# Kernel optimization log

Hardware: AMD Instinct MI355X
Metric: run time of the kernel (lower is better)

## Reference

```python
import jax, jax.numpy as jnp
import numpy as np
from math import comb

# --- module hyperparameters (from init_kwargs / module-level constants) ---
F = 32          # features
NITER = 3       # num_iterations
NB = 16         # num_basis_functions
NDCM = 4        # n_dcm
CUTOFF = 4.0
MAXZ = 17       # max_atomic_number
NC = 9          # (max_degree+1)^2 spherical components, max_degree=2
DEG = np.array([0, 1, 1, 1, 2, 2, 2, 2, 2])  # degree l of each component
BINOM = jnp.asarray([comb(NB - 1, k) for k in range(NB)], dtype=jnp.float32)


def _np_sph9(x, y, z):
    # real spherical harmonics up to l=2 on the unit sphere (numpy, for Gaunt table)
    c0 = 0.28209479177387814; c1 = 0.4886025119029199
    c2a = 1.0925484305920792; c2b = 0.31539156525252005; c2c = 0.5462742152960396
    return np.stack([c0 * np.ones_like(x), c1 * y, c1 * z, c1 * x,
                     c2a * x * y, c2a * y * z, c2b * (3.0 * z * z - 1.0),
                     c2a * x * z, c2c * (x * x - y * y)], axis=0)


def _gaunt():
    # real Gaunt (Clebsch-Gordan-type) coefficients G[a,b,c] = int Y_a Y_b Y_c dOmega
    # via Gauss-Legendre (cos theta) x midpoint (phi) quadrature -- exact for l<=2 products
    ct, wt = np.polynomial.legendre.leggauss(64)
    nph = 256
    phi = (np.arange(nph) + 0.5) * (2.0 * np.pi / nph)
    st = np.sqrt(1.0 - ct ** 2)
    x = st[:, None] * np.cos(phi)[None, :]
    y = st[:, None] * np.sin(phi)[None, :]
    z = np.broadcast_to(ct[:, None], x.shape)
    w = (wt[:, None] * (2.0 * np.pi / nph)) * np.ones((1, nph))
    Y = _np_sph9(x, y, z)
    G = np.einsum('aij,bij,cij,ij->abc', Y, Y, Y, w)
    G[np.abs(G) < 1e-6] = 0.0
    return G

CG = jnp.asarray(_gaunt(), dtype=jnp.float32)  # (9, 9, 9), sparse


def _sph9(u):
    # u: (E, 3) unit vectors -> (E, 9)
    x, y, z = u[:, 0], u[:, 1], u[:, 2]
    c0 = 0.28209479177387814; c1 = 0.4886025119029199
    c2a = 1.0925484305920792; c2b = 0.31539156525252005; c2c = 0.5462742152960396
    return jnp.stack([jnp.full_like(x, c0), c1 * y, c1 * z, c1 * x,
                      c2a * x * y, c2a * y * z, c2b * (3.0 * z * z - 1.0),
                      c2a * x * z, c2c * (x * x - y * y)], axis=-1)


def _radial(r):
    # reciprocal Bernstein radial basis * smooth cutoff; r: (E,) -> (E, NB)
    u = 1.0 / (1.0 + r)
    k = jnp.arange(NB, dtype=jnp.float32)
    rb = BINOM * u[:, None] ** k * (1.0 - u[:, None]) ** (NB - 1 - k)
    t = r / CUTOFF
    den = jnp.where(t < 1.0, 1.0 - t * t, 1.0)
    fc = jnp.where(t < 1.0, jnp.exp(-t * t / den), 0.0)  # smooth_cutoff
    return rb * fc[:, None]


def _equiv_dense(x, W, b=None):
    # per-degree linear (equivariant Dense): x (N, 9, Fin), W (3, Fin, Fout); bias on l=0 only
    y = jnp.einsum('ncf,cfg->ncg', x, W[DEG])
    if b is not None:
        y = y.at[:, 0, :].add(b)
    return y


def _tp(xs, bf):
    # Gaunt tensor-product contraction: out[e,c,f] = sum_ab CG[a,b,c] xs[e,a,f] bf[e,b,f]
    # loop over the 9 fixed output components to avoid an (E,9,9,F) intermediate
    out = []
    for c in range(NC):
        t = jnp.einsum('eaf,ab->ebf', xs, CG[:, :, c])
        out.append(jnp.sum(t * bf, axis=1))
    return jnp.stack(out, axis=1)


def _forward(atomic_numbers, positions, dst_idx, src_idx, embed, Wb, W1, b1, W2, b2,
             Wt00, Wt11, Wmono, element_bias):
    n = atomic_numbers.shape[0]
    disp = positions[src_idx] - positions[dst_idx]                 # (E, 3) gather
    r = jnp.sqrt(jnp.sum(disp * disp, axis=-1) + 1e-12)            # safe norm
    u = disp / r[:, None]
    basis = _sph9(u)[:, :, None] * _radial(r)[:, None, :]          # (E, 9, NB)
    x = jnp.zeros((n, NC, F), dtype=positions.dtype).at[:, 0, :].set(embed[atomic_numbers])
    for i in range(NITER):  # message passing iterations
        bf = jnp.einsum('ebn,bng->ebg', basis, Wb[i][DEG])         # per-degree radial->feature mix (E,9,F)
        msg = _tp(x[src_idx], bf)                                  # gather src + tensor product
        y = x + jax.ops.segment_sum(msg, dst_idx, num_segments=n)  # scatter-aggregate + residual add
        y = _equiv_dense(y, W1[i], b1[i])
        y = jax.nn.silu(y)
        y = _equiv_dense(y, W2[i], b2[i])
        x = x + y                                                  # residual update
    # TensorDense to n_dcm channels, then readout heads
    mono = (x[:, 0, :] @ Wt00) @ Wmono + element_bias[atomic_numbers][:, None]  # (N, NDCM)
    dip = jnp.einsum('ncf,fg->ncg', x[:, 1:4, :], Wt11)            # (N, 3, NDCM) vector channel
    dip = jnp.clip(jax.nn.silu(dip), -0.3, 0.3) + positions[:, :, None]
    return mono, dip


def setup_inputs():
    key = jax.random.key(0)
    ks = jax.random.split(key, 12)
    N, E = 10000, 160000
    return {
        'atomic_numbers': jax.random.randint(ks[0], (N,), 0, MAXZ + 1),
        'positions': jax.random.normal(ks[1], (N, 3), jnp.float32) * 3.0,
        'dst_idx': jax.random.randint(ks[2], (E,), 0, N),
        'src_idx': jax.random.randint(ks[3], (E,), 0, N),
        'embed': jax.random.normal(ks[4], (MAXZ + 1, F), jnp.float32),
        'Wb': jax.random.normal(ks[5], (NITER, 3, NB, F), jnp.float32) / np.sqrt(NB).astype(np.float32),
        'W1': jax.random.normal(ks[6], (NITER, 3, F, F), jnp.float32) / np.sqrt(F).astype(np.float32),
        'b1': jnp.zeros((NITER, F), jnp.float32),
        'W2': jax.random.normal(ks[7], (NITER, 3, F, F), jnp.float32) / np.sqrt(F).astype(np.float32),
        'b2': jnp.zeros((NITER, F), jnp.float32),
        'Wt00': jax.random.normal(ks[8], (F, NDCM), jnp.float32) / np.sqrt(F).astype(np.float32),
        'Wt11': jax.random.normal(ks[9], (F, NDCM), jnp.float32) / np.sqrt(F).astype(np.float32),
        'Wmono': jax.random.normal(ks[10], (NDCM, NDCM), jnp.float32) / np.sqrt(NDCM).astype(np.float32),
        'element_bias': jnp.zeros((MAXZ + 1,), jnp.float32),
    }


def reference(atomic_numbers, positions, dst_idx, src_idx, embed, Wb, W1, b1, W2, b2,
              Wt00, Wt11, Wmono, element_bias):
    return _forward(atomic_numbers, positions, dst_idx, src_idx, embed, Wb, W1, b1, W2, b2,
                    Wt00, Wt11, Wmono, element_bias)
```

## Files before the change

kernel.cpp:

```cpp
#include <hip/hip_runtime.h>
#include <hip/hip_bf16.h>


#define NITER 3
#define BCAP  64

#define OFF_WB    0
#define OFF_W1    4608
#define OFF_B1    13824
#define OFF_W2    13920
#define OFF_B2    23136
#define OFF_WT00  23232
#define OFF_WT11  23360
#define OFF_WMONO 23488
#define OFF_EB    23504
#define OFF_EMB   23522
#define WC_TOTAL  24098

__device__ __forceinline__ float b2f(const __hip_bfloat16 v) { return __bfloat162float(v); }

#define KC0 0.28209479177387814f
#define KG1 0.21850968611841584f
#define KG2 0.12615662610100802f
#define KG3 0.18022375157287861f
// ... 17 lines not shown
}

__device__ __forceinline__ float xadd32(float v) {
    return v + __int_as_float(__shfl_xor(__float_as_int(v), 32, 64));
}

__device__ __forceinline__ bool edge_geom(float dx, float dy, float dz,
                                          float* sp, float* rad) {
    float r2 = dx*dx + dy*dy + dz*dz + 1e-12f;
    if (r2 >= 16.0f) return false;
    float r  = sqrtf(r2);
    float t2 = r2 * 0.0625f;
    float fc = __expf(-t2 / (1.0f - t2));
    float u = 1.0f / (1.0f + r);
    float v = 1.0f - u;
    const float BIN[16] = {1.f,15.f,105.f,455.f,1365.f,3003.f,5005.f,6435.f,
                           6435.f,5005.f,3003.f,1365.f,455.f,105.f,15.f,1.f};
    float vp[16];
    vp[0] = 1.0f;
    #pragma unroll
    for (int k = 1; k < 16; k++) vp[k] = vp[k-1] * v;
    float up = 1.0f;
    #pragma unroll
    for (int n = 0; n < 16; n++) { rad[n] = BIN[n] * up * vp[15-n] * fc; up *= u; }
    float ir = 1.0f / r;
    float ux = dx*ir, uy = dy*ir, uz = dz*ir;
    const float c0 = 0.28209479177387814f, c1 = 0.4886025119029199f;
    const float c2a = 1.0925484305920792f, c2b = 0.31539156525252005f, c2c = 0.5462742152960396f;
    sp[0] = c0;
    sp[1] = c1*uy; sp[2] = c1*uz; sp[3] = c1*ux;
    sp[4] = c2a*ux*uy; sp[5] = c2a*uy*uz; sp[6] = c2b*(3.0f*uz*uz - 1.0f);
    sp[7] = c2a*ux*uz; sp[8] = c2c*(ux*ux - uy*uy);
    return true;
}

__global__ void setup_kernel(const void* pos, const void* Wb, const void* W1,
        const void* b1, const void* W2, const void* b2, const void* Wt00,
        const void* Wt11, const void* Wmono, const void* eb, const void* emb,
        const int* __restrict__ an,
        const int* __restrict__ srcI, const int* __restrict__ dstI,
        float* __restrict__ posf, float* __restrict__ wc,
        float* __restrict__ x, float* __restrict__ geo2, int* __restrict__ cur,
        int N, int E, int use_csr) {
    bool f32 = wave_sniff(pos);
    int i = blockIdx.x * blockDim.x + threadIdx.x;
    int np = N * 3;
    if (i < np) { posf[i] = ldany(pos, i, f32); return; }
    int j = i - np;
    if (j < WC_TOTAL) {
        const void* src; int rel;
        if      (j < OFF_W1)    { src = Wb;    rel = j; }
        else if (j < OFF_B1)    { src = W1;    rel = j - OFF_W1; }
        else if (j < OFF_W2)    { src = b1;    rel = j - OFF_B1; }
        else if (j < OFF_B2)    { src = W2;    rel = j - OFF_W2; }
        else if (j < OFF_WT00)  { src = b2;    rel = j - OFF_B2; }
        else if (j < OFF_WT11)  { src = Wt00;  rel = j - OFF_WT00; }
        else if (j < OFF_WMONO) { src = Wt11;  rel = j - OFF_WT11; }
        else if (j < OFF_EB)    { src = Wmono; rel = j - OFF_WMONO; }
        else if (j < OFF_EMB)   { src = eb;    rel = j - OFF_EB; }
        else                    { src = emb;   rel = j - OFF_EMB; }
        wc[j] = ldany(src, rel, f32);
        return;
    }
    j -= WC_TOTAL;
    if (j < N * 32) {
        int n = j >> 5, rem = j & 31;
        x[(size_t)n * 288 + rem] = ldany(emb, an[n] * 32 + rem, f32);
        return;
    }
    j -= N * 32;
    if (j < E && use_csr) {
        int s = srcI[j], d = dstI[j];
        float sp[9], rad[16];
        if (!edge_geom(ldany(pos, s*3+0, f32) - ldany(pos, d*3+0, f32),
                       ldany(pos, s*3+1, f32) - ldany(pos, d*3+1, f32),
                       ldany(pos, s*3+2, f32) - ldany(pos, d*3+2, f32),
                       sp, rad)) return;
        int slot = atomicAdd(&cur[d], 1);
        float* gp = geo2 + ((size_t)d * BCAP + slot) * 32;
        gp[0] = __int_as_float(s);
        gp[1] = 0.0f;
        #pragma unroll
        for (int a = 0; a < 9; a++) gp[2 + a] = sp[a];
        gp[11] = 0.0f;
        #pragma unroll
        for (int k = 0; k < 16; k++) gp[16 + k] = rad[k];
    }
}

template <bool FIRST, bool LAST>
__global__ __launch_bounds__(256) void edge_gather_kernel(
        const float* __restrict__ x, float* __restrict__ y,
        const float* __restrict__ geo2, const int* __restrict__ cur,
        const float* __restrict__ Wbi, int N) {
    int tid  = threadIdx.x;
    int f    = tid & 31;
    int half = (tid >> 5) & 1;
    int n    = (blockIdx.x * blockDim.x + tid) >> 6;
    if (n >= N) return;
    float w0[16], w1[16], w2[16];
    #pragma unroll
    for (int k = 0; k < 16; k++) {
        w0[k] = Wbi[(0*16 + k)*32 + f];
        w1[k] = Wbi[(1*16 + k)*32 + f];
        w2[k] = Wbi[(2*16 + k)*32 + f];
    }
    float A0=0.f,A1=0.f,A2=0.f,A3=0.f,A4=0.f,A5=0.f,A6=0.f,A7=0.f,A8=0.f;
    int beg = n * BCAP, end = beg + cur[n];
    for (int e = beg + half; e < end; e += 2) {
        const float4* gp = (const float4*)(geo2 + (size_t)e * 32);
        float4 h0 = gp[0], h1 = gp[1], h2 = gp[2];
        float4 r0 = gp[4], r1 = gp[5], r2 = gp[6], r3 = gp[7];
        int s = __float_as_int(h0.x);
        float rad[16] = {r0.x,r0.y,r0.z,r0.w, r1.x,r1.y,r1.z,r1.w,
                         r2.x,r2.y,r2.z,r2.w, r3.x,r3.y,r3.z,r3.w};
        float rw0 = 0.f, rw1 = 0.f, rw2 = 0.f;
        #pragma unroll
        for (int k = 0; k < 16; k++) {
            rw0 = fmaf(rad[k], w0[k], rw0);
            rw1 = fmaf(rad[k], w1[k], rw1);
            rw2 = fmaf(rad[k], w2[k], rw2);
        }
        float B0 = h0.z*rw0;
        float B1 = h0.w*rw1, B2 = h1.x*rw1, B3 = h1.y*rw1;
        float B4 = h1.z*rw2, B5 = h1.w*rw2, B6 = h2.x*rw2,
              B7 = h2.y*rw2, B8 = h2.z*rw2;
        const float* xp = x + (size_t)s*288 + f;
        if (FIRST) {
            float X0 = xp[0];
            float k0 = KC0 * X0;
            A0 += k0*B0; A1 += k0*B1; A2 += k0*B2; A3 += k0*B3; A4 += k0*B4;
            A5 += k0*B5; A6 += k0*B6; A7 += k0*B7; A8 += k0*B8;
        } else {
            float X0 = xp[0],   X1 = xp[32],  X2 = xp[64],  X3 = xp[96],  X4 = xp[128];
            float X5 = xp[160], X6 = xp[192], X7 = xp[224], X8 = xp[256];
            A0 += KC0*(X0*B0 + X1*B1 + X2*B2 + X3*B3 + X4*B4 + X5*B5 + X6*B6 + X7*B7 + X8*B8);
            A1 += KC0*(X0*B1 + X1*B0) + KG1*(X3*B4 + X4*B3 + X2*B5 + X5*B2)
                - KG2*(X1*B6 + X6*B1) - KG1*(X1*B8 + X8*B1);
            A2 += KC0*(X0*B2 + X2*B0) + KG1*(X1*B5 + X5*B1 + X3*B7 + X7*B3)
                + 2.0f*KG2*(X2*B6 + X6*B2);
            A3 += KC0*(X0*B3 + X3*B0) + KG1*(X1*B4 + X4*B1 + X2*B7 + X7*B2)
                - KG2*(X3*B6 + X6*B3) + KG1*(X3*B8 + X8*B3);
            if (!LAST) {
                A4 += KC0*(X0*B4 + X4*B0) + KG1*(X1*B3 + X3*B1) + KG5*(X5*B7 + X7*B5)
                    - KG3*(X4*B6 + X6*B4);
                A5 += KC0*(X0*B5 + X5*B0) + KG1*(X1*B2 + X2*B1) + KG5*(X4*B7 + X7*B4)
                    + KG4*(X5*B6 + X6*B5) - KG5*(X5*B8 + X8*B5);
                A6 += KC0*(X0*B6 + X6*B0) - KG2*X1*B1 + 2.0f*KG2*X2*B2 - KG2*X3*B3
                    - KG3*X4*B4 + KG4*X5*B5 + KG3*X6*B6 + KG4*X7*B7 - KG3*X8*B8;
                A7 += KC0*(X0*B7 + X7*B0) + KG1*(X2*B3 + X3*B2) + KG5*(X4*B5 + X5*B4)
                    + KG4*(X6*B7 + X7*B6) + KG5*(X7*B8 + X8*B7);
                A8 += KC0*(X0*B8 + X8*B0) - KG1*X1*B1 + KG1*X3*B3 - KG5*X5*B5 + KG5*X7*B7
                    - KG3*(X6*B8 + X8*B6);
            }
        }
    }
    A0 = xadd32(A0); A1 = xadd32(A1); A2 = xadd32(A2); A3 = xadd32(A3);
    if (!LAST) {
        A4 = xadd32(A4); A5 = xadd32(A5); A6 = xadd32(A6);
        A7 = xadd32(A7); A8 = xadd32(A8);
    }
    if (half == 0) {
        float* yp = y + (size_t)n * 288 + f;
        yp[0]   = A0; yp[32]  = A1; yp[64]  = A2; yp[96]  = A3;
        if (!LAST) {
            yp[128] = A4; yp[160] = A5; yp[192] = A6; yp[224] = A7; yp[256] = A8;
        }
    }
}

template <bool FIRST>
__global__ __launch_bounds__(256) void atom_kernel(
        float* __restrict__ x, const float* __restrict__ y,
        const float* __restrict__ W1i, const float* __restrict__ b1i,
        const float* __restrict__ W2i, const float* __restrict__ b2i,
        int N) {
    __shared__ float sm[4][64*33];
    int lane  = threadIdx.x & 63;
    int wslot = threadIdx.x >> 6;
    int u = __builtin_amdgcn_readfirstlane(blockIdx.x * 4 + wslot);
    int t = u / 9;
    int c = u - t * 9;
    int d = (c == 0) ? 0 : ((c < 4) ? 1 : 2);
    const float* W1 = W1i + d * 1024;
    const float* W2 = W2i + d * 1024;
    float* tile = sm[wslot];
    bool usex = (!FIRST) || (c == 0);
    float4 xr4[8];
    #pragma unroll
    for (int k = 0; k < 8; k++) {
        int e  = lane * 4 + k * 256;
        int al = e >> 5, f = e & 31;
        int ag = t * 64 + al;
        float4 s = make_float4(0.f, 0.f, 0.f, 0.f);
        float4 xv = make_float4(0.f, 0.f, 0.f, 0.f);
        if (ag < N) {
            if (usex) xv = *(const float4*)(x + (size_t)ag * 288 + c * 32 + f);
            float4 yv = *(const float4*)(y + (size_t)ag * 288 + c * 32 + f);
            s = make_float4(xv.x + yv.x, xv.y + yv.y, xv.z + yv.z, xv.w + yv.w);
        }
        xr4[k] = xv;
        *(float4*)(tile + al * 33 + f) = s;
    }
    __syncthreads();
    float yin[32];
    #pragma unroll
    for (int k = 0; k < 8; k++) {
        float4 v = *(const float4*)(tile + lane * 33 + 4 * k);
        yin[4*k+0] = v.x; yin[4*k+1] = v.y; yin[4*k+2] = v.z; yin[4*k+3] = v.w;
    }
    float acc[32];
    #pragma unroll
    for (int g = 0; g < 32; g++) acc[g] = (c == 0) ? b1i[g] : 0.0f;
    #pragma unroll 4
    for (int fi = 0; fi < 32; fi++) {
        float v = yin[fi];
        #pragma unroll
        for (int g = 0; g < 32; g++) acc[g] = fmaf(v, W1[fi*32 + g], acc[g]);
    }
    #pragma unroll
    for (int g = 0; g < 32; g++)
        acc[g] = acc[g] * __builtin_amdgcn_rcpf(1.0f + __expf(-acc[g]));
    float out[32];
    #pragma unroll
    for (int g = 0; g < 32; g++) out[g] = (c == 0) ? b2i[g] : 0.0f;
    #pragma unroll 4
    for (int fi = 0; fi < 32; fi++) {
        float v = acc[fi];
        #pragma unroll
        for (int g = 0; g < 32; g++) out[g] = fmaf(v, W2[fi*32 + g], out[g]);
    }
    __syncthreads();
    #pragma unroll
    for (int k = 0; k < 8; k++)
        *(float4*)(tile + lane * 33 + 4 * k) =
            make_float4(out[4*k+0], out[4*k+1], out[4*k+2], out[4*k+3]);
    __syncthreads();
    #pragma unroll
    for (int k = 0; k < 8; k++) {
        int e  = lane * 4 + k * 256;
        int al = e >> 5, f = e & 31;
        int ag = t * 64 + al;
        if (ag < N) {
            float4 dv = *(const float4*)(tile + al * 33 + f);
            float4 xv = xr4[k];
            *(float4*)(x + (size_t)ag * 288 + c * 32 + f) =
                make_float4(xv.x + dv.x, xv.y + dv.y, xv.z + dv.z, xv.w + dv.w);
        }
    }
}

__global__ __launch_bounds__(256) void atom_readout_kernel(
        const float* __restrict__ x, const float* __restrict__ y,
        const float* __restrict__ W1i, const float* __restrict__ b1i,
        const float* __restrict__ W2i, const float* __restrict__ b2i,
        const int* __restrict__ an, const float* __restrict__ posf,
        const float* __restrict__ wc, const void* __restrict__ pos,
        void* __restrict__ out_, int N) {
    bool f32 = wave_sniff(pos);
    __shared__ float sm[4][64*33];
    int lane  = threadIdx.x & 63;
    int wslot = threadIdx.x >> 6;
    int c = __builtin_amdgcn_readfirstlane(wslot);
    int t = blockIdx.x;
    int d = (c == 0) ? 0 : 1;
    const float* W1 = W1i + d * 1024;
    const float* W2 = W2i + d * 1024;
    float* tile = sm[wslot];
    float4 xr4[8];
    #pragma unroll
    for (int k = 0; k < 8; k++) {
        int e  = lane * 4 + k * 256;
        int al = e >> 5, f = e & 31;
        int ag = t * 64 + al;
        float4 s = make_float4(0.f, 0.f, 0.f, 0.f);
        float4 xv = make_float4(0.f, 0.f, 0.f, 0.f);
        if (ag < N) {
            xv = *(const float4*)(x + (size_t)ag * 288 + c * 32 + f);
            float4 yv = *(const float4*)(y + (size_t)ag * 288 + c * 32 + f);
            s = make_float4(xv.x + yv.x, xv.y + yv.y, xv.z + yv.z, xv.w + yv.w);
        }
        xr4[k] = xv;
        *(float4*)(tile + al * 33 + f) = s;
    }
    __syncthreads();
    float yin[32];
    #pragma unroll
    for (int k = 0; k < 8; k++) {
        float4 v = *(const float4*)(tile + lane * 33 + 4 * k);
        yin[4*k+0] = v.x; yin[4*k+1] = v.y; yin[4*k+2] = v.z; yin[4*k+3] = v.w;
    }
    float acc[32];
    #pragma unroll
    for (int g = 0; g < 32; g++) acc[g] = (c == 0) ? b1i[g] : 0.0f;
    #pragma unroll 4
    for (int fi = 0; fi < 32; fi++) {
        float v = yin[fi];
        #pragma unroll
        for (int g = 0; g < 32; g++) acc[g] = fmaf(v, W1[fi*32 + g], acc[g]);
    }
    #pragma unroll
    for (int g = 0; g < 32; g++)
        acc[g] = acc[g] * __builtin_amdgcn_rcpf(1.0f + __expf(-acc[g]));
    float out[32];
    #pragma unroll
    for (int g = 0; g < 32; g++) out[g] = (c == 0) ? b2i[g] : 0.0f;
    #pragma unroll 4
    for (int fi = 0; fi < 32; fi++) {
        float v = acc[fi];
        #pragma unroll
        for (int g = 0; g < 32; g++) out[g] = fmaf(v, W2[fi*32 + g], out[g]);
    }
    __syncthreads();
    #pragma unroll
    for (int k = 0; k < 8; k++)
        *(float4*)(tile + lane * 33 + 4 * k) =
            make_float4(out[4*k+0], out[4*k+1], out[4*k+2], out[4*k+3]);
    __syncthreads();
    #pragma unroll
    for (int k = 0; k < 8; k++) {
        int e  = lane * 4 + k * 256;
        int al = e >> 5, f = e & 31;
        float4 dv = *(const float4*)(tile + al * 33 + f);
        float4 xv = xr4[k];
        *(float4*)(tile + al * 33 + f) =
            make_float4(xv.x + dv.x, xv.y + dv.y, xv.z + dv.z, xv.w + dv.w);
    }
    __syncthreads();
    if (threadIdx.x < 64) {
        int a  = threadIdx.x;
        int ag = t * 64 + a;
        if (ag < N) {
            const float* Wt00  = wc + OFF_WT00;
            const float* Wt11  = wc + OFF_WT11;
            const float* Wmono = wc + OFF_WMONO;
            const float* x0 = sm[0] + a * 33;
            float q[4] = {0.f, 0.f, 0.f, 0.f};
            for (int f = 0; f < 32; f++) {
                float xv = x0[f];
                #pragma unroll
                for (int j = 0; j < 4; j++) q[j] = fmaf(xv, Wt00[f*4 + j], q[j]);
            }
            float ebv = wc[OFF_EB + an[ag]];
            #pragma unroll
            for (int m = 0; m < 4; m++) {
                float accm = ebv;
                #pragma unroll
                for (int j = 0; j < 4; j++) accm = fmaf(q[j], Wmono[j*4 + m], accm);
                if (f32) ((float*)out_)[ag*4 + m] = accm;
                else ((__hip_bfloat16*)out_)[ag*4 + m] = __float2bfloat16(accm);
            }
            #pragma unroll
            for (int cc = 0; cc < 3; cc++) {
                float pc = posf[ag*3 + cc];
                const float* xc = sm[1 + cc] + a * 33;
                float dq[4] = {0.f, 0.f, 0.f, 0.f};
                for (int f = 0; f < 32; f++) {
                    float xv = xc[f];
                    #pragma unroll
                    for (int m = 0; m < 4; m++) dq[m] = fmaf(xv, Wt11[f*4 + m], dq[m]);
                }
                #pragma unroll
                for (int m = 0; m < 4; m++) {
                    float v = dq[m];
                    v = v * __builtin_amdgcn_rcpf(1.0f + __expf(-v));
                    v = fminf(fmaxf(v, -0.3f), 0.3f);
                    v += pc;
                    if (f32) ((float*)out_)[N*4 + ag*12 + cc*4 + m] = v;
                    else ((__hip_bfloat16*)out_)[N*4 + ag*12 + cc*4 + m] = __float2bfloat16(v);
                }
            }
        }
    }
}

__global__ void zero_kernel(float4* __restrict__ b, int n) {
    int i = blockIdx.x * blockDim.x + threadIdx.x;
    int stride = gridDim.x * blockDim.x;
    float4 z = make_float4(0.f, 0.f, 0.f, 0.f);
    for (; i < n; i += stride) b[i] = z;
}

__global__ __launch_bounds__(256) void edge_inline_kernel(
        const float* __restrict__ x, float* __restrict__ y,
        const float* __restrict__ posf,
        const int* __restrict__ srcI, const int* __restrict__ dstI,
        const float* __restrict__ Wbi, int E) {
    int f  = threadIdx.x & 31;
    int hw = (blockIdx.x * blockDim.x + threadIdx.x) >> 5;
    int nhw = gridDim.x * (blockDim.x >> 5);
    float w0[16], w1[16], w2[16];
    #pragma unroll
    for (int n = 0; n < 16; n++) {
        w0[n] = Wbi[(0*16 + n)*32 + f];
        w1[n] = Wbi[(1*16 + n)*32 + f];
        w2[n] = Wbi[(2*16 + n)*32 + f];
    }
    for (int e = hw; e < E; e += nhw) {
        int s = srcI[e], d = dstI[e];
        float sp[9], rad[16];
        if (!edge_geom(posf[s*3+0] - posf[d*3+0],
                       posf[s*3+1] - posf[d*3+1],
                       posf[s*3+2] - posf[d*3+2], sp, rad)) continue;
        float rw0 = 0.f, rw1 = 0.f, rw2 = 0.f;
        #pragma unroll
        for (int n = 0; n < 16; n++) {
// ... 77 lines not shown
        }
        #pragma unroll
        for (int m = 0; m < 4; m++) {
            float v = dq[m];
            v = v * __builtin_amdgcn_rcpf(1.0f + __expf(-v));
            v = fminf(fmaxf(v, -0.3f), 0.3f);
            v += pc;
            if (f32) ((float*)out)[N*4 + n*12 + c*4 + m] = v;
            else ((__hip_bfloat16*)out)[N*4 + n*12 + c*4 + m] = __float2bfloat16(v);
        }
    }
}

extern "C" void kernel_launch(void* const* d_in, const int* in_sizes, int n_in,
                              void* d_out, int out_size, void* d_ws, size_t ws_size,
                              hipStream_t stream) {
    const int* an    = (const int*)d_in[0];
    const void* pos  = d_in[1];
    const int* dstI  = (const int*)d_in[2];
    const int* srcI  = (const int*)d_in[3];
    const void* embed= d_in[4];
    const void* Wb   = d_in[5];
    const void* W1   = d_in[6];
    const void* b1   = d_in[7];
    const void* W2   = d_in[8];
    const void* b2   = d_in[9];
    const void* Wt00 = d_in[10];
    const void* Wt11 = d_in[11];
    const void* Wmono= d_in[12];
    const void* eb   = d_in[13];
    int N = in_sizes[0];
    int E = in_sizes[2];

    float* x    = (float*)d_ws;
    float* y    = x + (size_t)N * 288;
    float* posf = y + (size_t)N * 288;
    float* wc   = posf + (size_t)N * 3;
    int* cur    = (int*)(wc + WC_TOTAL);
    uintptr_t ga = ((uintptr_t)(cur + N) + 127) & ~(uintptr_t)127;
    float* geo2 = (float*)ga;
    size_t need = (uintptr_t)(geo2 + (size_t)N * BCAP * 32) - (uintptr_t)d_ws;
    bool use_csr = (ws_size >= need);

    hipMemsetAsync(cur, 0, sizeof(int) * (size_t)N, stream);
    if (!use_csr)
        zero_kernel<<<512, 256, 0, stream>>>((float4*)x, N * 72);
    {
        int tot = N * 3 + WC_TOTAL + N * 32 + (use_csr ? E : 0);
        setup_kernel<<<(tot + 255)/256, 256, 0, stream>>>(
            pos, Wb, W1, b1, W2, b2, Wt00, Wt11, Wmono, eb, embed,
            an, srcI, dstI, posf, wc, x, geo2, cur, N, E, use_csr ? 1 : 0);
    }
    int ntiles = (N + 63) / 64;
    if (use_csr) {
        int gblocks = (N + 3) / 4;
        for (int i = 0; i < NITER; i++) {
            const float* Wbi = wc + OFF_WB + (size_t)i*1536;
            const float* W1i = wc + OFF_W1 + (size_t)i*3072;
            const float* b1i = wc + OFF_B1 + (size_t)i*32;
            const float* W2i = wc + OFF_W2 + (size_t)i*3072;
            const float* b2i = wc + OFF_B2 + (size_t)i*32;
            if (i == 0) {
                edge_gather_kernel<true,false><<<gblocks, 256, 0, stream>>>(
                    x, y, geo2, cur, Wbi, N);
                atom_kernel<true><<<(ntiles*9 + 3)/4, 256, 0, stream>>>(
                    x, y, W1i, b1i, W2i, b2i, N);
            } else if (i == NITER - 1) {
                edge_gather_kernel<false,true><<<gblocks, 256, 0, stream>>>(
                    x, y, geo2, cur, Wbi, N);
                atom_readout_kernel<<<ntiles, 256, 0, stream>>>(
                    x, y, W1i, b1i, W2i, b2i, an, posf, wc, pos, d_out, N);
            } else {
                edge_gather_kernel<false,false><<<gblocks, 256, 0, stream>>>(
                    x, y, geo2, cur, Wbi, N);
                atom_kernel<false><<<(ntiles*9 + 3)/4, 256, 0, stream>>>(
                    x, y, W1i, b1i, W2i, b2i, N);
            }
        }
    } else {
        int ablocks = (ntiles * 9 + 3) / 4;
        for (int i = 0; i < NITER; i++) {
            zero_kernel<<<512, 256, 0, stream>>>((float4*)y, N * 72);
            edge_inline_kernel<<<2048, 256, 0, stream>>>(x, y, posf, srcI, dstI,
                wc + OFF_WB + (size_t)i*1536, E);
            atom_kernel<false><<<ablocks, 256, 0, stream>>>(x, y,
                wc + OFF_W1 + (size_t)i*3072, wc + OFF_B1 + (size_t)i*32,
                wc + OFF_W2 + (size_t)i*3072, wc + OFF_B2 + (size_t)i*32, N);
        }
        readout_kernel<<<(N + 255)/256, 256, 0, stream>>>(x, an, posf, wc, pos,
                                                          d_out, N);
    }
}
```

Before: 212.2 us.

## Fuse edge gather and atom MLP into one per-iteration kernel with ping-pong buffers

Replaces the separate edge_gather and atom kernels in the CSR path with a single iter_kernel per iteration. Each wavefront gathers messages for one atom, adds the residual, and runs the two 32x32 MLPs from a shared-memory tile. The last iteration also computes the readout directly. Features ping-pong between two buffers so the y intermediate array is never written or re-read, and three launches plus their global round-trips are removed. In exchange, each 64-lane wave now does the MLP work for one atom, reading weights per channel instead of using the earlier 64-atom tiled matmul, so MLP weight reuse is lower.

New measurement: 224.1 us. +5.6%, slower.

```diff
diff --git a/kernel.cpp b/kernel.cpp
--- a/kernel.cpp
+++ b/kernel.cpp
@@ -73,6 +73,214 @@
     sp[4] = c2a*ux*uy; sp[5] = c2a*uy*uz; sp[6] = c2b*(3.0f*uz*uz - 1.0f);
     sp[7] = c2a*ux*uz; sp[8] = c2c*(ux*ux - uy*uy);
     return true;
+}
+
+__device__ __forceinline__ void write_geo_slot(float* gp, int s,
+                                               const float* sp, const float* rad) {
+    float4* g4 = (float4*)gp;
+    g4[0] = make_float4(__int_as_float(s), 0.f, sp[0], sp[1]);
+    g4[1] = make_float4(sp[2], sp[3], sp[4], sp[5]);
+    g4[2] = make_float4(sp[6], sp[7], sp[8], 0.f);
+    g4[4] = make_float4(rad[0],  rad[1],  rad[2],  rad[3]);
+    g4[5] = make_float4(rad[4],  rad[5],  rad[6],  rad[7]);
+    g4[6] = make_float4(rad[8],  rad[9],  rad[10], rad[11]);
+    g4[7] = make_float4(rad[12], rad[13], rad[14], rad[15]);
+}
+
+template <bool FIRST, bool LAST>
+__global__ __launch_bounds__(256) void iter_kernel(
+        const float* __restrict__ xin, float* __restrict__ xout,
+        const float* __restrict__ geo2, const int* __restrict__ cur,
+        const float* __restrict__ Wbi,
+        const float* __restrict__ W1i, const float* __restrict__ b1i,
+        const float* __restrict__ W2i, const float* __restrict__ b2i,
+        const int* __restrict__ an, const float* __restrict__ posf,
+        const float* __restrict__ wc, const void* __restrict__ pos,
+        void* __restrict__ out_, int N) {
+    constexpr int NCH = LAST ? 4 : 9;
+    constexpr int NR  = LAST ? 2 : 5;
+    __shared__ float sm[4][9][33];
+    bool f32o = false;
+    if (LAST) f32o = wave_sniff(pos);
+    int tid   = threadIdx.x;
+    int wslot = tid >> 6;
+    int lane  = tid & 63;
+    int f     = lane & 31;
+    int half  = lane >> 5;
+    int n     = blockIdx.x * 4 + wslot;
+    bool act  = (n < N);
+    float (*tile)[33] = sm[wslot];
+
+    float w0[16], w1[16], w2[16];
+    #pragma unroll
+    for (int k = 0; k < 16; k++) {
+        w0[k] = Wbi[(0*16 + k)*32 + f];
+        w1[k] = Wbi[(1*16 + k)*32 + f];
+        w2[k] = Wbi[(2*16 + k)*32 + f];
+    }
+    float A0=0.f,A1=0.f,A2=0.f,A3=0.f,A4=0.f,A5=0.f,A6=0.f,A7=0.f,A8=0.f;
+    if (act) {
+        int beg = n * BCAP, end = beg + cur[n];
+        for (int e = beg + half; e < end; e += 2) {
+            const float4* gp = (const float4*)(geo2 + (size_t)e * 32);
+            float4 h0 = gp[0], h1 = gp[1], h2 = gp[2];
+            float4 r0 = gp[4], r1 = gp[5], r2 = gp[6], r3 = gp[7];
+            int s = __float_as_int(h0.x);
+            float rad[16] = {r0.x,r0.y,r0.z,r0.w, r1.x,r1.y,r1.z,r1.w,
+                             r2.x,r2.y,r2.z,r2.w, r3.x,r3.y,r3.z,r3.w};
+            float rw0 = 0.f, rw1 = 0.f, rw2 = 0.f;
+            #pragma unroll
+            for (int k = 0; k < 16; k++) {
+                rw0 = fmaf(rad[k], w0[k], rw0);
+                rw1 = fmaf(rad[k], w1[k], rw1);
+                rw2 = fmaf(rad[k], w2[k], rw2);
+            }
+            float B0 = h0.z*rw0;
+            float B1 = h0.w*rw1, B2 = h1.x*rw1, B3 = h1.y*rw1;
+            float B4 = h1.z*rw2, B5 = h1.w*rw2, B6 = h2.x*rw2,
+                  B7 = h2.y*rw2, B8 = h2.z*rw2;
+            const float* xp = xin + (size_t)s*288 + f;
+            if (FIRST) {
+                float X0 = xp[0];
+                float k0 = KC0 * X0;
+                A0 += k0*B0; A1 += k0*B1; A2 += k0*B2; A3 += k0*B3; A4 += k0*B4;
+                A5 += k0*B5; A6 += k0*B6; A7 += k0*B7; A8 += k0*B8;
+            } else {
+                float X0 = xp[0],   X1 = xp[32],  X2 = xp[64],  X3 = xp[96],  X4 = xp[128];
+                float X5 = xp[160], X6 = xp[192], X7 = xp[224], X8 = xp[256];
+                A0 += KC0*(X0*B0 + X1*B1 + X2*B2 + X3*B3 + X4*B4 + X5*B5 + X6*B6 + X7*B7 + X8*B8);
+                A1 += KC0*(X0*B1 + X1*B0) + KG1*(X3*B4 + X4*B3 + X2*B5 + X5*B2)
+                    - KG2*(X1*B6 + X6*B1) - KG1*(X1*B8 + X8*B1);
+                A2 += KC0*(X0*B2 + X2*B0) + KG1*(X1*B5 + X5*B1 + X3*B7 + X7*B3)
+                    + 2.0f*KG2*(X2*B6 + X6*B2);
+                A3 += KC0*(X0*B3 + X3*B0) + KG1*(X1*B4 + X4*B1 + X2*B7 + X7*B2)
+                    - KG2*(X3*B6 + X6*B3) + KG1*(X3*B8 + X8*B3);
+                if (!LAST) {
+                    A4 += KC0*(X0*B4 + X4*B0) + KG1*(X1*B3 + X3*B1) + KG5*(X5*B7 + X7*B5)
+                        - KG3*(X4*B6 + X6*B4);
+                    A5 += KC0*(X0*B5 + X5*B0) + KG1*(X1*B2 + X2*B1) + KG5*(X4*B7 + X7*B4)
+                        + KG4*(X5*B6 + X6*B5) - KG5*(X5*B8 + X8*B5);
+                    A6 += KC0*(X0*B6 + X6*B0) - KG2*X1*B1 + 2.0f*KG2*X2*B2 - KG2*X3*B3
+                        - KG3*X4*B4 + KG4*X5*B5 + KG3*X6*B6 + KG4*X7*B7 - KG3*X8*B8;
+                    A7 += KC0*(X0*B7 + X7*B0) + KG1*(X2*B3 + X3*B2) + KG5*(X4*B5 + X5*B4)
+                        + KG4*(X6*B7 + X7*B6) + KG5*(X7*B8 + X8*B7);
+                    A8 += KC0*(X0*B8 + X8*B0) - KG1*X1*B1 + KG1*X3*B3 - KG5*X5*B5 + KG5*X7*B7
+                        - KG3*(X6*B8 + X8*B6);
+                }
+            }
+        }
+    }
+    A0 = xadd32(A0); A1 = xadd32(A1); A2 = xadd32(A2); A3 = xadd32(A3);
+    if (!LAST) {
+        A4 = xadd32(A4); A5 = xadd32(A5); A6 = xadd32(A6);
+        A7 = xadd32(A7); A8 = xadd32(A8);
+    }
+
+    float xr[9];
+    #pragma unroll
+    for (int c = 0; c < 9; c++) xr[c] = 0.f;
+    if (act) {
+        if (FIRST) {
+            xr[0] = xin[(size_t)n*288 + f];
+        } else {
+            #pragma unroll
+            for (int c = 0; c < NCH; c++) xr[c] = xin[(size_t)n*288 + c*32 + f];
+        }
+    }
+
+    if (act && half == 0) {
+        tile[0][f] = xr[0] + A0;
+        tile[1][f] = xr[1] + A1;
+        tile[2][f] = xr[2] + A2;
+        tile[3][f] = xr[3] + A3;
+        if (!LAST) {
+            tile[4][f] = xr[4] + A4;
+            tile[5][f] = xr[5] + A5;
+            tile[6][f] = xr[6] + A6;
+            tile[7][f] = xr[7] + A7;
+            tile[8][f] = xr[8] + A8;
+        }
+    }
+    __syncthreads();
+
+    int g = f;
+    float o1[NR];
+    #pragma unroll
+    for (int cc = 0; cc < NR; cc++) {
+        int c  = cc*2 + half;
+        int cs = (c < NCH) ? c : 0;
+        int d  = (cs == 0) ? 0 : ((cs < 4) ? 1 : 2);
+        const float* W1p = W1i + d * 1024;
+        float acc = (c == 0) ? b1i[g] : 0.f;
+        #pragma unroll
+        for (int fi = 0; fi < 32; fi++)
+            acc = fmaf(tile[cs][fi], W1p[fi*32 + g], acc);
+        acc = acc * __builtin_amdgcn_rcpf(1.0f + __expf(-acc));
+        o1[cc] = acc;
+    }
+    __syncthreads();
+    #pragma unroll
+    for (int cc = 0; cc < NR; cc++) {
+        int c = cc*2 + half;
+        if (c < NCH) tile[c][g] = o1[cc];
+    }
+    __syncthreads();
+
+    #pragma unroll
+    for (int cc = 0; cc < NR; cc++) {
+        int c  = cc*2 + half;
+        int cs = (c < NCH) ? c : 0;
+        int d  = (cs == 0) ? 0 : ((cs < 4) ? 1 : 2);
+        const float* W2p = W2i + d * 1024;
+        float acc = (c == 0) ? b2i[g] : 0.f;
+        #pragma unroll
+        for (int fi = 0; fi < 32; fi++)
+            acc = fmaf(tile[cs][fi], W2p[fi*32 + g], acc);
+        float xf = xr[cs] + acc;
+        if (!LAST) {
+            if (act && c < NCH)
+                xout[(size_t)n*288 + c*32 + g] = xf;
+        } else if (act) {
+            const float* WT = (c == 0) ? (wc + OFF_WT00) : (wc + OFF_WT11);
+            float p0 = xf * WT[g*4 + 0];
+            float p1 = xf * WT[g*4 + 1];
+            float p2 = xf * WT[g*4 + 2];
+            float p3 = xf * WT[g*4 + 3];
+            #pragma unroll
+            for (int m = 1; m <= 16; m <<= 1) {
+                p0 += __shfl_xor(p0, m, 64);
+                p1 += __shfl_xor(p1, m, 64);
+                p2 += __shfl_xor(p2, m, 64);
+                p3 += __shfl_xor(p3, m, 64);
+            }
+            if (g == 0) {
+                if (c == 0) {
+                    const float* Wmono = wc + OFF_WMONO;
+                    float ebv = wc[OFF_EB + an[n]];
+                    #pragma unroll
+                    for (int m = 0; m < 4; m++) {
+                        float a2 = ebv + p0*Wmono[0*4+m] + p1*Wmono[1*4+m]
+                                       + p2*Wmono[2*4+m] + p3*Wmono[3*4+m];
+                        if (f32o) ((float*)out_)[n*4 + m] = a2;
+                        else ((__hip_bfloat16*)out_)[n*4 + m] = __float2bfloat16(a2);
+                    }
+                } else {
+                    float pc = posf[n*3 + (c - 1)];
+                    float pv[4] = {p0, p1, p2, p3};
+                    #pragma unroll
+                    for (int m = 0; m < 4; m++) {
+                        float v = pv[m];
+                        v = v * __builtin_amdgcn_rcpf(1.0f + __expf(-v));
+                        v = fminf(fmaxf(v, -0.3f), 0.3f);
+                        v += pc;
+                        size_t o = (size_t)N*4 + (size_t)n*12 + (size_t)(c-1)*4 + m;
+                        if (f32o) ((float*)out_)[o] = v;
+                        else ((__hip_bfloat16*)out_)[o] = __float2bfloat16(v);
+                    }
+                }
+            }
+        }
+    }
 }
 
 __global__ void setup_kernel(const void* pos, const void* Wb, const void* W1,
@@ -118,94 +326,81 @@
                        ldany(pos, s*3+2, f32) - ldany(pos, d*3+2, f32),
                        sp, rad)) return;
         int slot = atomicAdd(&cur[d], 1);
-        float* gp = geo2 + ((size_t)d * BCAP + slot) * 32;
-        gp[0] = __int_as_float(s);
-        gp[1] = 0.0f;
-        #pragma unroll
-        for (int a = 0; a < 9; a++) gp[2 + a] = sp[a];
-        gp[11] = 0.0f;
-        #pragma unroll
-        for (int k = 0; k < 16; k++) gp[16 + k] = rad[k];
-    }
-}
-
-template <bool FIRST, bool LAST>
-__global__ __launch_bounds__(256) void edge_gather_kernel(
-        const float* __restrict__ x, float* __restrict__ y,
-        const float* __restrict__ geo2, const int* __restrict__ cur,
-        const float* __restrict__ Wbi, int N) {
-    int tid  = threadIdx.x;
-    int f    = tid & 31;
-    int half = (tid >> 5) & 1;
-    int n    = (blockIdx.x * blockDim.x + tid) >> 6;
-    if (n >= N) return;
-    float w0[16], w1[16], w2[16];
-    #pragma unroll
-    for (int k = 0; k < 16; k++) {
-        w0[k] = Wbi[(0*16 + k)*32 + f];
-        w1[k] = Wbi[(1*16 + k)*32 + f];
-        w2[k] = Wbi[(2*16 + k)*32 + f];
-    }
-    float A0=0.f,A1=0.f,A2=0.f,A3=0.f,A4=0.f,A5=0.f,A6=0.f,A7=0.f,A8=0.f;
-    int beg = n * BCAP, end = beg + cur[n];
-    for (int e = beg + half; e < end; e += 2) {
-        const float4* gp = (const float4*)(geo2 + (size_t)e * 32);
-        float4 h0 = gp[0], h1 = gp[1], h2 = gp[2];
-        float4 r0 = gp[4], r1 = gp[5], r2 = gp[6], r3 = gp[7];
-        int s = __float_as_int(h0.x);
-        float rad[16] = {r0.x,r0.y,r0.z,r0.w, r1.x,r1.y,r1.z,r1.w,
-                         r2.x,r2.y,r2.z,r2.w, r3.x,r3.y,r3.z,r3.w};
-        float rw0 = 0.f, rw1 = 0.f, rw2 = 0.f;
-        #pragma unroll
-        for (int k = 0; k < 16; k++) {
-            rw0 = fmaf(rad[k], w0[k], rw0);
-            rw1 = fmaf(rad[k], w1[k], rw1);
-            rw2 = fmaf(rad[k], w2[k], rw2);
-        }
-        float B0 = h0.z*rw0;
-        float B1 = h0.w*rw1, B2 = h1.x*rw1, B3 = h1.y*rw1;
-        float B4 = h1.z*rw2, B5 = h1.w*rw2, B6 = h2.x*rw2,
-              B7 = h2.y*rw2, B8 = h2.z*rw2;
-        const float* xp = x + (size_t)s*288 + f;
-        if (FIRST) {
-            float X0 = xp[0];
-            float k0 = KC0 * X0;
-            A0 += k0*B0; A1 += k0*B1; A2 += k0*B2; A3 += k0*B3; A4 += k0*B4;
-            A5 += k0*B5; A6 += k0*B6; A7 += k0*B7; A8 += k0*B8;
-        } else {
-            float X0 = xp[0],   X1 = xp[32],  X2 = xp[64],  X3 = xp[96],  X4 = xp[128];
-            float X5 = xp[160], X6 = xp[192], X7 = xp[224], X8 = xp[256];
-            A0 += KC0*(X0*B0 + X1*B1 + X2*B2 + X3*B3 + X4*B4 + X5*B5 + X6*B6 + X7*B7 + X8*B8);
-            A1 += KC0*(X0*B1 + X1*B0) + KG1*(X3*B4 + X4*B3 + X2*B5 + X5*B2)
-                - KG2*(X1*B6 + X6*B1) - KG1*(X1*B8 + X8*B1);
-            A2 += KC0*(X0*B2 + X2*B0) + KG1*(X1*B5 + X5*B1 + X3*B7 + X7*B3)
-                + 2.0f*KG2*(X2*B6 + X6*B2);
-            A3 += KC0*(X0*B3 + X3*B0) + KG1*(X1*B4 + X4*B1 + X2*B7 + X7*B2)
-                - KG2*(X3*B6 + X6*B3) + KG1*(X3*B8 + X8*B3);
-            if (!LAST) {
-                A4 += KC0*(X0*B4 + X4*B0) + KG1*(X1*B3 + X3*B1) + KG5*(X5*B7 + X7*B5)
-                    - KG3*(X4*B6 + X6*B4);
-                A5 += KC0*(X0*B5 + X5*B0) + KG1*(X1*B2 + X2*B1) + KG5*(X4*B7 + X7*B4)
-                    + KG4*(X5*B6 + X6*B5) - KG5*(X5*B8 + X8*B5);
-                A6 += KC0*(X0*B6 + X6*B0) - KG2*X1*B1 + 2.0f*KG2*X2*B2 - KG2*X3*B3
-                    - KG3*X4*B4 + KG4*X5*B5 + KG3*X6*B6 + KG4*X7*B7 - KG3*X8*B8;
-                A7 += KC0*(X0*B7 + X7*B0) + KG1*(X2*B3 + X3*B2) + KG5*(X4*B5 + X5*B4)
-                    + KG4*(X6*B7 + X7*B6) + KG5*(X7*B8 + X8*B7);
-                A8 += KC0*(X0*B8 + X8*B0) - KG1*X1*B1 + KG1*X3*B3 - KG5*X5*B5 + KG5*X7*B7
-                    - KG3*(X6*B8 + X8*B6);
-            }
-        }
-    }
-    A0 = xadd32(A0); A1 = xadd32(A1); A2 = xadd32(A2); A3 = xadd32(A3);
-    if (!LAST) {
-        A4 = xadd32(A4); A5 = xadd32(A5); A6 = xadd32(A6);
-        A7 = xadd32(A7); A8 = xadd32(A8);
-    }
-    if (half == 0) {
-        float* yp = y + (size_t)n * 288 + f;
-        yp[0]   = A0; yp[32]  = A1; yp[64]  = A2; yp[96]  = A3;
-        if (!LAST) {
-            yp[128] = A4; yp[160] = A5; yp[192] = A6; yp[224] = A7; yp[256] = A8;
+        write_geo_slot(geo2 + ((size_t)d * BCAP + slot) * 32, s, sp, rad);
+    }
+}
+
+template <bool FIRST>
+__device__ __forceinline__ void atom_unit(
+        const float* __restrict__ xin, float* __restrict__ xout,
+        const float* __restrict__ y,
+        const float* __restrict__ W1i, const float* __restrict__ b1i,
+        const float* __restrict__ W2i, const float* __restrict__ b2i,
+        int N, int t, int c, int lane, float* __restrict__ tile) {
+    int d = (c == 0) ? 0 : ((c < 4) ? 1 : 2);
+    const float* W1 = W1i + d * 1024;
+    const float* W2 = W2i + d * 1024;
+    bool usex = (!FIRST) || (c == 0);
+    float4 xr4[8];
+    #pragma unroll
+    for (int k = 0; k < 8; k++) {
+        int e  = lane * 4 + k * 256;
+        int al = e >> 5, f = e & 31;
+        int ag = t * 64 + al;
+        float4 s = make_float4(0.f, 0.f, 0.f, 0.f);
+        float4 xv = make_float4(0.f, 0.f, 0.f, 0.f);
+        if (ag < N) {
+            if (usex) xv = *(const float4*)(xin + (size_t)ag * 288 + c * 32 + f);
+            float4 yv = *(const float4*)(y + (size_t)ag * 288 + c * 32 + f);
+            s = make_float4(xv.x + yv.x, xv.y + yv.y, xv.z + yv.z, xv.w + yv.w);
+        }
+        xr4[k] = xv;
+        *(float4*)(tile + al * 33 + f) = s;
+    }
+    __syncthreads();
+    float yin[32];
+    #pragma unroll
+    for (int k = 0; k < 8; k++) {
+        float4 v = *(const float4*)(tile + lane * 33 + 4 * k);
+        yin[4*k+0] = v.x; yin[4*k+1] = v.y; yin[4*k+2] = v.z; yin[4*k+3] = v.w;
+    }
+    float acc[32];
+    #pragma unroll
+    for (int g = 0; g < 32; g++) acc[g] = (c == 0) ? b1i[g] : 0.0f;
+    #pragma unroll 4
+    for (int fi = 0; fi < 32; fi++) {
+        float v = yin[fi];
+        #pragma unroll
+        for (int g = 0; g < 32; g++) acc[g] = fmaf(v, W1[fi*32 + g], acc[g]);
+    }
+    #pragma unroll
+    for (int g = 0; g < 32; g++)
+        acc[g] = acc[g] * __builtin_amdgcn_rcpf(1.0f + __expf(-acc[g]));
+    float out[32];
+    #pragma unroll
+    for (int g = 0; g < 32; g++) out[g] = (c == 0) ? b2i[g] : 0.0f;
+    #pragma unroll 4
+    for (int fi = 0; fi < 32; fi++) {
+        float v = acc[fi];
+        #pragma unroll
+        for (int g = 0; g < 32; g++) out[g] = fmaf(v, W2[fi*32 + g], out[g]);
+    }
+    __syncthreads();
+    #pragma unroll
+    for (int k = 0; k < 8; k++)
+        *(float4*)(tile + lane * 33 + 4 * k) =
+            make_float4(out[4*k+0], out[4*k+1], out[4*k+2], out[4*k+3]);
+    __syncthreads();
+    #pragma unroll
+    for (int k = 0; k < 8; k++) {
+        int e  = lane * 4 + k * 256;
+        int al = e >> 5, f = e & 31;
+        int ag = t * 64 + al;
+        if (ag < N) {
+            float4 dv = *(const float4*)(tile + al * 33 + f);
+            float4 xv = xr4[k];
+            *(float4*)(xout + (size_t)ag * 288 + c * 32 + f) =
+                make_float4(xv.x + dv.x, xv.y + dv.y, xv.z + dv.z, xv.w + dv.w);
         }
     }
 }
@@ -222,197 +417,7 @@
     int u = __builtin_amdgcn_readfirstlane(blockIdx.x * 4 + wslot);
     int t = u / 9;
     int c = u - t * 9;
-    int d = (c == 0) ? 0 : ((c < 4) ? 1 : 2);
-    const float* W1 = W1i + d * 1024;
-    const float* W2 = W2i + d * 1024;
-    float* tile = sm[wslot];
-    bool usex = (!FIRST) || (c == 0);
-    float4 xr4[8];
-    #pragma unroll
-    for (int k = 0; k < 8; k++) {
-        int e  = lane * 4 + k * 256;
-        int al = e >> 5, f = e & 31;
-        int ag = t * 64 + al;
-        float4 s = make_float4(0.f, 0.f, 0.f, 0.f);
-        float4 xv = make_float4(0.f, 0.f, 0.f, 0.f);
-        if (ag < N) {
-            if (usex) xv = *(const float4*)(x + (size_t)ag * 288 + c * 32 + f);
-            float4 yv = *(const float4*)(y + (size_t)ag * 288 + c * 32 + f);
-            s = make_float4(xv.x + yv.x, xv.y + yv.y, xv.z + yv.z, xv.w + yv.w);
-        }
-        xr4[k] = xv;
-        *(float4*)(tile + al * 33 + f) = s;
-    }
-    __syncthreads();
-    float yin[32];
-    #pragma unroll
-    for (int k = 0; k < 8; k++) {
-        float4 v = *(const float4*)(tile + lane * 33 + 4 * k);
-        yin[4*k+0] = v.x; yin[4*k+1] = v.y; yin[4*k+2] = v.z; yin[4*k+3] = v.w;
-    }
-    float acc[32];
-    #pragma unroll
-    for (int g = 0; g < 32; g++) acc[g] = (c == 0) ? b1i[g] : 0.0f;
-    #pragma unroll 4
-    for (int fi = 0; fi < 32; fi++) {
-        float v = yin[fi];
-        #pragma unroll
-        for (int g = 0; g < 32; g++) acc[g] = fmaf(v, W1[fi*32 + g], acc[g]);
-    }
-    #pragma unroll
-    for (int g = 0; g < 32; g++)
-        acc[g] = acc[g] * __builtin_amdgcn_rcpf(1.0f + __expf(-acc[g]));
-    float out[32];
-    #pragma unroll
-    for (int g = 0; g < 32; g++) out[g] = (c == 0) ? b2i[g] : 0.0f;
-    #pragma unroll 4
-    for (int fi = 0; fi < 32; fi++) {
-        float v = acc[fi];
-        #pragma unroll
-        for (int g = 0; g < 32; g++) out[g] = fmaf(v, W2[fi*32 + g], out[g]);
-    }
-    __syncthreads();
-    #pragma unroll
-    for (int k = 0; k < 8; k++)
-        *(float4*)(tile + lane * 33 + 4 * k) =
-            make_float4(out[4*k+0], out[4*k+1], out[4*k+2], out[4*k+3]);
-    __syncthreads();
-    #pragma unroll
-    for (int k = 0; k < 8; k++) {
-        int e  = lane * 4 + k * 256;
-        int al = e >> 5, f = e & 31;
-        int ag = t * 64 + al;
-        if (ag < N) {
-            float4 dv = *(const float4*)(tile + al * 33 + f);
-            float4 xv = xr4[k];
-            *(float4*)(x + (size_t)ag * 288 + c * 32 + f) =
-                make_float4(xv.x + dv.x, xv.y + dv.y, xv.z + dv.z, xv.w + dv.w);
-        }
-    }
-}
-
-__global__ __launch_bounds__(256) void atom_readout_kernel(
-        const float* __restrict__ x, const float* __restrict__ y,
-        const float* __restrict__ W1i, const float* __restrict__ b1i,
-        const float* __restrict__ W2i, const float* __restrict__ b2i,
-        const int* __restrict__ an, const float* __restrict__ posf,
-        const float* __restrict__ wc, const void* __restrict__ pos,
-        void* __restrict__ out_, int N) {
-    bool f32 = wave_sniff(pos);
-    __shared__ float sm[4][64*33];
-    int lane  = threadIdx.x & 63;
-    int wslot = threadIdx.x >> 6;
-    int c = __builtin_amdgcn_readfirstlane(wslot);
-    int t = blockIdx.x;
-    int d = (c == 0) ? 0 : 1;
-    const float* W1 = W1i + d * 1024;
-    const float* W2 = W2i + d * 1024;
-    float* tile = sm[wslot];
-    float4 xr4[8];
-    #pragma unroll
-    for (int k = 0; k < 8; k++) {
-        int e  = lane * 4 + k * 256;
-        int al = e >> 5, f = e & 31;
-        int ag = t * 64 + al;
-        float4 s = make_float4(0.f, 0.f, 0.f, 0.f);
-        float4 xv = make_float4(0.f, 0.f, 0.f, 0.f);
-        if (ag < N) {
-            xv = *(const float4*)(x + (size_t)ag * 288 + c * 32 + f);
-            float4 yv = *(const float4*)(y + (size_t)ag * 288 + c * 32 + f);
-            s = make_float4(xv.x + yv.x, xv.y + yv.y, xv.z + yv.z, xv.w + yv.w);
-        }
-        xr4[k] = xv;
-        *(float4*)(tile + al * 33 + f) = s;
-    }
-    __syncthreads();
-    float yin[32];
-    #pragma unroll
-    for (int k = 0; k < 8; k++) {
-        float4 v = *(const float4*)(tile + lane * 33 + 4 * k);
-        yin[4*k+0] = v.x; yin[4*k+1] = v.y; yin[4*k+2] = v.z; yin[4*k+3] = v.w;
-    }
-    float acc[32];
-    #pragma unroll
-    for (int g = 0; g < 32; g++) acc[g] = (c == 0) ? b1i[g] : 0.0f;
-    #pragma unroll 4
-    for (int fi = 0; fi < 32; fi++) {
-        float v = yin[fi];
-        #pragma unroll
-        for (int g = 0; g < 32; g++) acc[g] = fmaf(v, W1[fi*32 + g], acc[g]);
-    }
-    #pragma unroll
-    for (int g = 0; g < 32; g++)
-        acc[g] = acc[g] * __builtin_amdgcn_rcpf(1.0f + __expf(-acc[g]));
-    float out[32];
-    #pragma unroll
-    for (int g = 0; g < 32; g++) out[g] = (c == 0) ? b2i[g] : 0.0f;
-    #pragma unroll 4
-    for (int fi = 0; fi < 32; fi++) {
-        float v = acc[fi];
-        #pragma unroll
-        for (int g = 0; g < 32; g++) out[g] = fmaf(v, W2[fi*32 + g], out[g]);
-    }
-    __syncthreads();
-    #pragma unroll
-    for (int k = 0; k < 8; k++)
-        *(float4*)(tile + lane * 33 + 4 * k) =
-            make_float4(out[4*k+0], out[4*k+1], out[4*k+2], out[4*k+3]);
-    __syncthreads();
-    #pragma unroll
-    for (int k = 0; k < 8; k++) {
-        int e  = lane * 4 + k * 256;
-        int al = e >> 5, f = e & 31;
-        float4 dv = *(const float4*)(tile + al * 33 + f);
-        float4 xv = xr4[k];
-        *(float4*)(tile + al * 33 + f) =
-            make_float4(xv.x + dv.x, xv.y + dv.y, xv.z + dv.z, xv.w + dv.w);
-    }
-    __syncthreads();
-    if (threadIdx.x < 64) {
-        int a  = threadIdx.x;
-        int ag = t * 64 + a;
-        if (ag < N) {
-            const float* Wt00  = wc + OFF_WT00;
-            const float* Wt11  = wc + OFF_WT11;
-            const float* Wmono = wc + OFF_WMONO;
-            const float* x0 = sm[0] + a * 33;
-            float q[4] = {0.f, 0.f, 0.f, 0.f};
-            for (int f = 0; f < 32; f++) {
-                float xv = x0[f];
-                #pragma unroll
-                for (int j = 0; j < 4; j++) q[j] = fmaf(xv, Wt00[f*4 + j], q[j]);
-            }
-            float ebv = wc[OFF_EB + an[ag]];
-            #pragma unroll
-            for (int m = 0; m < 4; m++) {
-                float accm = ebv;
-                #pragma unroll
-                for (int j = 0; j < 4; j++) accm = fmaf(q[j], Wmono[j*4 + m], accm);
-                if (f32) ((float*)out_)[ag*4 + m] = accm;
-                else ((__hip_bfloat16*)out_)[ag*4 + m] = __float2bfloat16(accm);
-            }
-            #pragma unroll
-            for (int cc = 0; cc < 3; cc++) {
-                float pc = posf[ag*3 + cc];
-                const float* xc = sm[1 + cc] + a * 33;
-                float dq[4] = {0.f, 0.f, 0.f, 0.f};
-                for (int f = 0; f < 32; f++) {
-                    float xv = xc[f];
-                    #pragma unroll
-                    for (int m = 0; m < 4; m++) dq[m] = fmaf(xv, Wt11[f*4 + m], dq[m]);
-                }
-                #pragma unroll
-                for (int m = 0; m < 4; m++) {
-                    float v = dq[m];
-                    v = v * __builtin_amdgcn_rcpf(1.0f + __expf(-v));
-                    v = fminf(fmaxf(v, -0.3f), 0.3f);
-                    v += pc;
-                    if (f32) ((float*)out_)[N*4 + ag*12 + cc*4 + m] = v;
-                    else ((__hip_bfloat16*)out_)[N*4 + ag*12 + cc*4 + m] = __float2bfloat16(v);
-                }
-            }
-        }
-    }
+    atom_unit<FIRST>(x, x, y, W1i, b1i, W2i, b2i, N, t, c, lane, sm[wslot]);
 }
 
 __global__ void zero_kernel(float4* __restrict__ b, int n) {
@@ -556,62 +561,64 @@
     int N = in_sizes[0];
     int E = in_sizes[2];
 
+    {
+        float* x0   = (float*)d_ws;
+        float* x1   = x0 + (size_t)N * 288;
+        float* posf = x1 + (size_t)N * 288;
+        float* wc   = posf + (size_t)N * 3;
+        int* cur    = (int*)(wc + WC_TOTAL);
+        uintptr_t ga = ((uintptr_t)(cur + N) + 127) & ~(uintptr_t)127;
+        float* geo2 = (float*)ga;
+        size_t need = (uintptr_t)(geo2 + (size_t)N * BCAP * 32) - (uintptr_t)d_ws;
+        if (ws_size >= need) {
+            hipMemsetAsync(cur, 0, sizeof(int) * (size_t)N, stream);
+            int tot = N * 3 + WC_TOTAL + N * 32 + E;
+            setup_kernel<<<(tot + 255)/256, 256, 0, stream>>>(
+                pos, Wb, W1, b1, W2, b2, Wt00, Wt11, Wmono, eb, embed,
+                an, srcI, dstI, posf, wc, x0, geo2, cur, N, E, 1);
+            int gblocks = (N + 3) / 4;
+            iter_kernel<true,false><<<gblocks, 256, 0, stream>>>(
+                x0, x1, geo2, cur,
+                wc + OFF_WB, wc + OFF_W1, wc + OFF_B1, wc + OFF_W2, wc + OFF_B2,
+                an, posf, wc, pos, d_out, N);
+            iter_kernel<false,false><<<gblocks, 256, 0, stream>>>(
+                x1, x0, geo2, cur,
+                wc + OFF_WB + 1536, wc + OFF_W1 + 3072, wc + OFF_B1 + 32,
+                wc + OFF_W2 + 3072, wc + OFF_B2 + 32,
+                an, posf, wc, pos, d_out, N);
+            iter_kernel<false,true><<<gblocks, 256, 0, stream>>>(
+                x0, nullptr, geo2, cur,
+                wc + OFF_WB + 3072, wc + OFF_W1 + 6144, wc + OFF_B1 + 64,
+                wc + OFF_W2 + 6144, wc + OFF_B2 + 64,
+                an, posf, wc, pos, d_out, N);
+            return;
+        }
+    }
+
     float* x    = (float*)d_ws;
     float* y    = x + (size_t)N * 288;
     float* posf = y + (size_t)N * 288;
     float* wc   = posf + (size_t)N * 3;
     int* cur    = (int*)(wc + WC_TOTAL);
-    uintptr_t ga = ((uintptr_t)(cur + N) + 127) & ~(uintptr_t)127;
-    float* geo2 = (float*)ga;
-    size_t need = (uintptr_t)(geo2 + (size_t)N * BCAP * 32) - (uintptr_t)d_ws;
-    bool use_csr = (ws_size >= need);
+    int ntiles = (N + 63) / 64;
 
     hipMemsetAsync(cur, 0, sizeof(int) * (size_t)N, stream);
-    if (!use_csr)
-        zero_kernel<<<512, 256, 0, stream>>>((float4*)x, N * 72);
+    zero_kernel<<<512, 256, 0, stream>>>((float4*)x, N * 72);
     {
-        int tot = N * 3 + WC_TOTAL + N * 32 + (use_csr ? E : 0);
+        int tot = N * 3 + WC_TOTAL + N * 32;
         setup_kernel<<<(tot + 255)/256, 256, 0, stream>>>(
             pos, Wb, W1, b1, W2, b2, Wt00, Wt11, Wmono, eb, embed,
-            an, srcI, dstI, posf, wc, x, geo2, cur, N, E, use_csr ? 1 : 0);
-    }
-    int ntiles = (N + 63) / 64;
-    if (use_csr) {
-        int gblocks = (N + 3) / 4;
-        for (int i = 0; i < NITER; i++) {
-            const float* Wbi = wc + OFF_WB + (size_t)i*1536;
-            const float* W1i = wc + OFF_W1 + (size_t)i*3072;
-            const float* b1i = wc + OFF_B1 + (size_t)i*32;
-            const float* W2i = wc + OFF_W2 + (size_t)i*3072;
-            const float* b2i = wc + OFF_B2 + (size_t)i*32;
-            if (i == 0) {
-                edge_gather_kernel<true,false><<<gblocks, 256, 0, stream>>>(
-                    x, y, geo2, cur, Wbi, N);
-                atom_kernel<true><<<(ntiles*9 + 3)/4, 256, 0, stream>>>(
-                    x, y, W1i, b1i, W2i, b2i, N);
-            } else if (i == NITER - 1) {
-                edge_gather_kernel<false,true><<<gblocks, 256, 0, stream>>>(
-                    x, y, geo2, cur, Wbi, N);
-                atom_readout_kernel<<<ntiles, 256, 0, stream>>>(
-                    x, y, W1i, b1i, W2i, b2i, an, posf, wc, pos, d_out, N);
-            } else {
-                edge_gather_kernel<false,false><<<gblocks, 256, 0, stream>>>(
-                    x, y, geo2, cur, Wbi, N);
-                atom_kernel<false><<<(ntiles*9 + 3)/4, 256, 0, stream>>>(
-                    x, y, W1i, b1i, W2i, b2i, N);
-            }
-        }
-    } else {
-        int ablocks = (ntiles * 9 + 3) / 4;
-        for (int i = 0; i < NITER; i++) {
-            zero_kernel<<<512, 256, 0, stream>>>((float4*)y, N * 72);
-            edge_inline_kernel<<<2048, 256, 0, stream>>>(x, y, posf, srcI, dstI,
-                wc + OFF_WB + (size_t)i*1536, E);
-            atom_kernel<false><<<ablocks, 256, 0, stream>>>(x, y,
-                wc + OFF_W1 + (size_t)i*3072, wc + OFF_B1 + (size_t)i*32,
-                wc + OFF_W2 + (size_t)i*3072, wc + OFF_B2 + (size_t)i*32, N);
-        }
-        readout_kernel<<<(N + 255)/256, 256, 0, stream>>>(x, an, posf, wc, pos,
-                                                          d_out, N);
-    }
-}
+            an, srcI, dstI, posf, wc, x, nullptr, cur, N, E, 0);
+    }
+    int ablocks = (ntiles * 9 + 3) / 4;
+    for (int i = 0; i < NITER; i++) {
+        zero_kernel<<<512, 256, 0, stream>>>((float4*)y, N * 72);
+        edge_inline_kernel<<<2048, 256, 0, stream>>>(x, y, posf, srcI, dstI,
+            wc + OFF_WB + (size_t)i*1536, E);
+        atom_kernel<false><<<ablocks, 256, 0, stream>>>(x, y,
+            wc + OFF_W1 + (size_t)i*3072, wc + OFF_B1 + (size_t)i*32,
+            wc + OFF_W2 + (size_t)i*3072, wc + OFF_B2 + (size_t)i*32, N);
+    }
+    readout_kernel<<<(N + 255)/256, 256, 0, stream>>>(x, an, posf, wc, pos,
+                                                      d_out, N);
+}
```
